# Kernel tuning notes

Hardware: AMD Instinct MI355X
Metric: run time of the kernel (lower is better)

## Reference

```python
import jax, jax.numpy as jnp
import numpy as np

B, CIN, H, W = 64, 3, 96, 96
COUT, KH, KW = 96, 5, 5
STRIDE, PAD = 2, 2
LR, K_TOP, DELTA, P_LEB = 0.02, 2, -0.4, 3.0
PREC = 1e-30


def im2col(x):
    # torch nn.Unfold ordering: channel-major (C, kh, kw) flattened -> [B, C*KH*KW, L]
    xp = jnp.pad(x, ((0, 0), (0, 0), (PAD, PAD), (PAD, PAD)))
    Hout = (H + 2 * PAD - KH) // STRIDE + 1
    Wout = (W + 2 * PAD - KW) // STRIDE + 1
    cols = []
    for i in range(KH):  # small fixed kernel loop (25 slices)
        for j in range(KW):
            cols.append(xp[:, :, i:i + STRIDE * (Hout - 1) + 1:STRIDE,
                           j:j + STRIDE * (Wout - 1) + 1:STRIDE])
    patches = jnp.stack(cols, axis=2)  # [B, C, KH*KW, Hout, Wout]
    return patches.reshape(x.shape[0], CIN * KH * KW, Hout * Wout)  # [B, K, L]


def setup_inputs() -> dict:
    key = jax.random.key(0)
    k1, k2 = jax.random.split(key)
    inp = jax.random.normal(k1, (B, CIN, H, W), dtype=jnp.float32)
    weight = jax.random.normal(k2, (COUT, CIN, KH, KW), dtype=jnp.float32)  # init.normal_
    return {"input": inp, "weight": weight}


def reference(input, weight):
    # standard conv forward (F.conv2d, no bias)
    out = jax.lax.conv_general_dilated(
        input, weight, (STRIDE, STRIDE), [(PAD, PAD), (PAD, PAD)],
        dimension_numbers=("NCHW", "OIHW", "NCHW"))

    # --- Krotov-Hopfield Hebbian update ---
    pre = im2col(input)                      # [B, K, L]
    Wm = weight.reshape(COUT, -1)            # [O, K]
    # sign(W) * |W|^(p-1) @ pre
    tot = jnp.einsum("ok,bkl->bol", jnp.sign(Wm) * jnp.abs(Wm) ** (P_LEB - 1.0), pre)  # [B,O,L]

    Bn, _, L = tot.shape
    _, idx = jax.lax.top_k(tot.transpose(0, 2, 1), K_TOP)   # [B, L, k] over output channels
    vals = jnp.concatenate([jnp.ones((1,), tot.dtype),
                            jnp.full((K_TOP - 1,), DELTA, tot.dtype)])  # top-1 -> 1.0, rest -> delta
    act = jnp.zeros((Bn, L, COUT), tot.dtype).at[
        jnp.arange(Bn)[:, None, None], jnp.arange(L)[None, :, None], idx
    ].set(jnp.broadcast_to(vals, (Bn, L, K_TOP)))
    act = act.transpose(0, 2, 1)             # [B, O, L]

    yx = jnp.einsum("bol,bkl->ok", act, pre) / L          # mean over L, sum over batch
    yy = (act * tot).sum(0).mean(1)                        # [O]
    ds = yx - yy[:, None] * Wm                             # [O, K]
    nc = jnp.maximum(jnp.max(jnp.abs(ds)), PREC)
    new_weight = weight + LR * (ds / nc).reshape(weight.shape)
    return out, new_weight
```

## Files before the change

kernel.cpp:

```cpp
#include <hip/hip_runtime.h>

#define B_     64
#define HW_    96
#define COUT_  96
#define KK_    75
#define KPAD   96
#define HOUT_  48
#define L_     2304
#define LR_    0.02f
#define DELTA_ -0.4f
#define OUT_ELEMS (B_*COUT_*L_)
#define XPITCH 100
#define XSLOTS 3368
#define C2     192
#define NPART  (B_*12)
#define ROW    (COUT_*KK_ + COUT_)
#define X2P    99
#define X2N    (33*X2P)

typedef __attribute__((ext_vector_type(8))) short short8v;
typedef __attribute__((ext_vector_type(4))) float float4v;
typedef __attribute__((ext_vector_type(4))) unsigned uint4v;

__device__ __forceinline__ unsigned short f2bf(float f) {
  unsigned u = __float_as_uint(f);
  u += 0x7fff + ((u >> 16) & 1);
  return (unsigned short)(u >> 16);
}

__device__ __forceinline__ void ins2(float v, int o, float& v1, int& o1,
                                     float& v2, int& o2) {
  bool b1 = (v > v1) || (v == v1 && o < o1);
  bool b2 = (v > v2) || (v == v2 && o < o2);
  if (b1)      { v2 = v1; o2 = o1; v1 = v; o1 = o; }
  else if (b2) { v2 = v;  o2 = o; }
}

__global__ __launch_bounds__(256) void k0_prep(const float* __restrict__ w,
                                               unsigned short* __restrict__ wbf) {
  int i = blockIdx.x * 256 + threadIdx.x;
  if (i >= 192 * KPAD) return;
  int row = i / KPAD, k = i - row * KPAD;
  float v = 0.0f;
  if (k < KK_) {
    float ww = w[(row % COUT_) * KK_ + k];
    v = (row < COUT_) ? ww : ww * fabsf(ww);
  }
  wbf[i] = f2bf(v);
}

__device__ __forceinline__ int wswz(int blk, int row) {
  return (blk < 8) ? (blk ^ (row & 7)) : (blk ^ (row & 3));
}

__global__ __launch_bounds__(256, 3) void k1_mfma(
    const float* __restrict__ x, const unsigned short* __restrict__ wbf,
    float* __restrict__ out, float4* __restrict__ top2)
{
  __shared__ __align__(16) unsigned short wlds[192 * KPAD];
  __shared__ __align__(16) float xs[XSLOTS];
  const int tid = threadIdx.x;
  const int lane = tid & 63, wq = tid >> 6;
  const int b = blockIdx.y;
  const int bx = blockIdx.x;
  const int col = lane & 15, g = lane >> 4;
  const float* xb = x + (size_t)b * (3 * HW_ * HW_);

  #pragma unroll
  for (int i = 0; i < 9; ++i) {
    int id = tid + i * 256;
    int row = id / 12, blk = id - row * 12;
    uint4v v = *(const uint4v*)(wbf + row * KPAD + blk * 8);
    *(uint4v*)((char*)wlds + row * 192 + wswz(blk, row) * 16) = v;
  }

  const int ihbase = 8 * bx - 2;
  #pragma unroll
  for (int i = 0; i < 14; ++i) {
    int idx = tid + i * 256;
    if (idx < XSLOTS) {
      int row = idx / XPITCH, iwr = idx - row * XPITCH;
      int c = row / 11, ihr = row - c * 11;
      int ih = ihbase + ihr, iw = iwr - 2;
      float v = 0.0f;
      if (c < 3 && (unsigned)ih < (unsigned)HW_ && (unsigned)iw < (unsigned)HW_)
        v = xb[(c * HW_ + ih) * HW_ + iw];
      xs[idx] = v;
    }
  }

  int offs[12][2];
  {
    const int base_fl = wq * 200 + 2 * col;
    #pragma unroll
    for (int kt = 0; kt < 3; ++kt)
      #pragma unroll
      for (int e2 = 0; e2 < 4; ++e2)
        #pragma unroll
        for (int par = 0; par < 2; ++par) {
          int k = kt * 32 + g * 8 + 2 * e2 + par;
          int c = k / 25, r = k - 25 * c, ki = r / 5, kj = r - 5 * ki;
          int fl = (k < KK_) ? base_fl + (c * 11 + ki) * XPITCH + kj
                             : 33 * XPITCH;
          offs[kt * 4 + e2][par] = fl * 4;
        }
  }

  __syncthreads();

  short8v bfr[3][3];
  #pragma unroll
  for (int nt = 0; nt < 3; ++nt)
    #pragma unroll
    for (int kt = 0; kt < 3; ++kt) {
      uint4v pk;
      #pragma unroll
      for (int e2 = 0; e2 < 4; ++e2) {
        const float* p0 = (const float*)((const char*)xs + offs[kt*4+e2][0]);
        const float* p1 = (const float*)((const char*)xs + offs[kt*4+e2][1]);
        float v0 = p0[nt * 32];
        float v1 = p1[nt * 32];
        pk[e2] = (unsigned)f2bf(v0) | ((unsigned)f2bf(v1) << 16);
      }
      bfr[nt][kt] = __builtin_bit_cast(short8v, pk);
    }

  const int lrow0 = (4 * bx + wq) * 48;
  float4v acc[3][6];

  #pragma unroll
  for (int nt = 0; nt < 3; ++nt)
    #pragma unroll
    for (int mt = 0; mt < 6; ++mt) acc[nt][mt] = (float4v)(0.0f);
  #pragma unroll
  for (int kt = 0; kt < 3; ++kt) {
    const int blk = kt * 4 + g;
    #pragma unroll
    for (int mt = 0; mt < 6; ++mt) {
      const int row = mt * 16 + col;
      short8v afr = *(const short8v*)(
          (const char*)wlds + row * 192 + wswz(blk, row) * 16);
      #pragma unroll
      for (int nt = 0; nt < 3; ++nt)
        acc[nt][mt] = __builtin_amdgcn_mfma_f32_16x16x32_bf16(
            afr, bfr[nt][kt], acc[nt][mt], 0, 0, 0);
    }
  }
  #pragma unroll
  for (int mt = 0; mt < 6; ++mt)
    #pragma unroll
    for (int r = 0; r < 4; ++r) {
      const int ch = mt * 16 + g * 4 + r;
      float* op = out + ((size_t)b * COUT_ + ch) * L_ + lrow0 + col;
      #pragma unroll
      for (int nt = 0; nt < 3; ++nt) op[nt * 16] = acc[nt][mt][r];
    }

  #pragma unroll
  for (int nt = 0; nt < 3; ++nt)
    #pragma unroll
    for (int mt = 0; mt < 6; ++mt) acc[nt][mt] = (float4v)(0.0f);
  #pragma unroll
  for (int kt = 0; kt < 3; ++kt) {
    const int blk = kt * 4 + g;
    #pragma unroll
    for (int mt = 0; mt < 6; ++mt) {
      const int row = 96 + mt * 16 + col;
      short8v afr = *(const short8v*)(
          (const char*)wlds + row * 192 + wswz(blk, row) * 16);
      #pragma unroll
      for (int nt = 0; nt < 3; ++nt)
        acc[nt][mt] = __builtin_amdgcn_mfma_f32_16x16x32_bf16(
            afr, bfr[nt][kt], acc[nt][mt], 0, 0, 0);
    }
  }
  #pragma unroll
  for (int nt = 0; nt < 3; ++nt) {
    float v1 = -3.0e38f, v2 = -3.0e38f;
    int o1 = 0x7fffffff, o2 = 0x7fffffff;
    #pragma unroll
    for (int mt = 0; mt < 6; ++mt)
      #pragma unroll
      for (int r = 0; r < 4; ++r)
        ins2(acc[nt][mt][r], mt * 16 + g * 4 + r, v1, o1, v2, o2);
    #pragma unroll
    for (int st = 0; st < 2; ++st) {
      const int d = (st == 0) ? 16 : 32;
      float bv1 = __shfl_xor(v1, d, 64);
      int   bo1 = __shfl_xor(o1, d, 64);
      float bv2 = __shfl_xor(v2, d, 64);
      int   bo2 = __shfl_xor(o2, d, 64);
      ins2(bv1, bo1, v1, o1, v2, o2);
      ins2(bv2, bo2, v1, o1, v2, o2);
    }
    if (g == 0)
      top2[(size_t)b * L_ + lrow0 + nt * 16 + col] =
          make_float4(v1, __int_as_float(o1), v2, __int_as_float(o2));
  }
}

__global__ __launch_bounds__(256, 2) void k2_gemm(
    const float* __restrict__ x, const float4* __restrict__ top2,
    float* __restrict__ part)
{
  __shared__ __align__(16) unsigned short actS[COUT_ * C2];
  __shared__ __align__(16) unsigned short preT[COUT_ * C2];
  __shared__ __align__(16) unsigned short xsb[X2N + 13];
  __shared__ float yyS[COUT_];
  const int tid = threadIdx.x;
  const int b = blockIdx.y;
  const int bx = blockIdx.x;
  const int l0 = bx * C2;
  const float* xb = x + (size_t)b * (3 * HW_ * HW_);

  {
    float4* a4 = (float4*)actS;
    #pragma unroll
    for (int i = 0; i < 9; ++i) a4[tid + i * 256] = make_float4(0, 0, 0, 0);
    float4* p4 = (float4*)((char*)preT + KK_ * (C2 * 2));
    if (tid < 252) {
      p4[2 * tid]     = make_float4(0, 0, 0, 0);
      p4[2 * tid + 1] = make_float4(0, 0, 0, 0);
    }
    if (tid < COUT_) yyS[tid] = 0.0f;
  }

  const int ihb2 = 8 * bx - 2;
  #pragma unroll
  for (int i = 0; i < 13; ++i) {
    int idx = tid + i * 256;
    if (idx < X2N) {
      int row = idx / X2P, iwr = idx - row * X2P;
      int c = row / 11, ihr = row - c * 11;
      int ih = ihb2 + ihr, iw = iwr - 2;
      float v = 0.0f;
      if (c < 3 && (unsigned)ih < (unsigned)HW_ && (unsigned)iw < (unsigned)HW_)
        v = xb[(c * HW_ + ih) * HW_ + iw];
      xsb[idx] = f2bf(v);
    }
  }
  __syncthreads();

  if (tid < C2) {
    const int pos = tid;
    const int ohr = pos / HOUT_, ow = pos - ohr * HOUT_;
    const int pblk = pos >> 3, plo = (pos & 7) << 1;
    const unsigned short* xl = xsb + (2 * ohr) * X2P + 2 * ow;
    #pragma unroll
    for (int c = 0; c < 3; ++c)
      #pragma unroll
      for (int ki = 0; ki < 5; ++ki)
        #pragma unroll
        for (int kj = 0; kj < 5; ++kj) {
          int k = c * 25 + ki * 5 + kj;
          unsigned short v = xl[(c * 11 + ki) * X2P + kj];
          *(unsigned short*)((char*)preT +
              k * (C2 * 2) + ((pblk ^ (k & 7)) << 4) + plo) = v;
        }
    float4 t2 = top2[(size_t)b * L_ + l0 + pos];
    int o1 = __float_as_int(t2.y), o2 = __float_as_int(t2.w);
    *(unsigned short*)((char*)actS +
        o1 * (C2 * 2) + ((pblk ^ (o1 & 7)) << 4) + plo) = 0x3F80;
    *(unsigned short*)((char*)actS +
        o2 * (C2 * 2) + ((pblk ^ (o2 & 7)) << 4) + plo) = f2bf(DELTA_);
    atomicAdd(&yyS[o1], t2.x);
    atomicAdd(&yyS[o2], DELTA_ * t2.z);
  }
  __syncthreads();

  const int lane = tid & 63, w = tid >> 6;
  const int col = lane & 15, g = lane >> 4;
  const int mb = (w >> 1) * 48, nb = (w & 1) * 48;

  float4v acc[3][3];
  #pragma unroll
  for (int mt = 0; mt < 3; ++mt)
    #pragma unroll
    for (int nt = 0; nt < 3; ++nt) acc[mt][nt] = (float4v)(0.0f);

  #pragma unroll
  for (int kt = 0; kt < 6; ++kt) {
    short8v a[3], bf[3];
    #pragma unroll
    for (int mt = 0; mt < 3; ++mt) {
      int row = mb + mt * 16 + col;
      a[mt] = *(const short8v*)((char*)actS + row * (C2 * 2) +
                                (((kt * 4 + g) ^ (row & 7)) << 4));
    }
    #pragma unroll
    for (int nt = 0; nt < 3; ++nt) {
      int row = nb + nt * 16 + col;
      bf[nt] = *(const short8v*)((char*)preT + row * (C2 * 2) +
                                 (((kt * 4 + g) ^ (row & 7)) << 4));
    }
    #pragma unroll
    for (int mt = 0; mt < 3; ++mt)
      #pragma unroll
      for (int nt = 0; nt < 3; ++nt)
        acc[mt][nt] = __builtin_amdgcn_mfma_f32_16x16x32_bf16(
            a[mt], bf[nt], acc[mt][nt], 0, 0, 0);
  }
  __syncthreads();

  float* prow = part + (size_t)(b * 12 + bx) * ROW;
  #pragma unroll
  for (int mt = 0; mt < 3; ++mt)
    #pragma unroll
    for (int nt = 0; nt < 3; ++nt)
      #pragma unroll
      for (int r = 0; r < 4; ++r) {
        int m = mb + mt * 16 + g * 4 + r;
        int n = nb + nt * 16 + col;
        if (n < KK_) prow[m * KK_ + n] = acc[mt][nt][r];
      }
  if (tid < COUT_) prow[COUT_ * KK_ + tid] = yyS[tid];
}

__global__ __launch_bounds__(256) void k3_reduce(
    const float* __restrict__ part, float* __restrict__ finals)
{
  __shared__ float red[4][64];
  const int e = blockIdx.x * 64 + (threadIdx.x & 63);
  const int seg = threadIdx.x >> 6;
  float s = 0.0f;
  for (int p = seg * (NPART / 4); p < (seg + 1) * (NPART / 4); ++p)
    s += part[(size_t)p * ROW + e];
  red[seg][threadIdx.x & 63] = s;
  __syncthreads();
  if (seg == 0) {
    int ll = threadIdx.x & 63;
    finals[e] = (red[0][ll] + red[1][ll]) + (red[2][ll] + red[3][ll]);
  }
}

__global__ __launch_bounds__(256) void k4_finalize(
    const float* __restrict__ w, const float* __restrict__ finals,
    float* __restrict__ outw)
{
  __shared__ float dsS[COUT_ * KK_];
  __shared__ float wmax[4];
  __shared__ float ncS;
  const int tid = threadIdx.x;
  float m = 0.0f;
  for (int i = tid; i < COUT_ * KK_; i += 256) {
    int o = i / KK_;
    float d = finals[i] - finals[COUT_ * KK_ + o] * w[i];
    dsS[i] = d;
    m = fmaxf(m, fabsf(d));
  }
  #pragma unroll
  for (int s = 32; s > 0; s >>= 1) m = fmaxf(m, __shfl_xor(m, s, 64));
  if ((tid & 63) == 0) wmax[tid >> 6] = m;
  __syncthreads();
  if (tid == 0) {
    float n = fmaxf(fmaxf(wmax[0], wmax[1]), fmaxf(wmax[2], wmax[3]));
    ncS = fmaxf(n, 1e-30f);
  }
  __syncthreads();
  const float scale = LR_ / ncS;
  for (int i = tid; i < COUT_ * KK_; i += 256) {
    outw[i] = w[i] + scale * dsS[i];
  }
}

extern "C" void kernel_launch(void* const* d_in, const int* in_sizes, int n_in,
                              void* d_out, int out_size, void* d_ws, size_t ws_size,
                              hipStream_t stream) {
  (void)in_sizes; (void)n_in; (void)out_size; (void)ws_size;
  const float* x = (const float*)d_in[0];
  const float* w = (const float*)d_in[1];
  float* out  = (float*)d_out;
  float* outw = out + OUT_ELEMS;

  unsigned short* wbf = (unsigned short*)d_ws;
  float4* top2 = (float4*)((char*)d_ws + 192 * KPAD * 2);
  float*  part = (float*)((char*)top2 + (size_t)B_ * L_ * sizeof(float4));
  float*  finals = part + (size_t)NPART * ROW;

  k0_prep   <<<dim3((192 * KPAD + 255) / 256), 256, 0, stream>>>(w, wbf);
  k1_mfma   <<<dim3(12, B_), 256, 0, stream>>>(x, wbf, out, top2);
  k2_gemm   <<<dim3(12, B_), 256, 0, stream>>>(x, top2, part);
  k3_reduce <<<dim3(ROW / 64), 256, 0, stream>>>(part, finals);
  k4_finalize<<<dim3(1), 256, 0, stream>>>(w, finals, outw);
}
```

Baseline: 115.8 us.

## Stage conv output through LDS for coalesced stores and split partial reduction

The conv output tile in k1 is now computed after the top-2 pass and transposed through shared memory (reusing the weight LDS region), so each channel row is written with contiguous float4 stores instead of scattered 4-byte stores. The partial-sum reduction is split into two kernels: a 2D grid that reduces groups of 96 partials in parallel, then a small fold kernel. This is meant to improve global write coalescing and raise parallelism in the reduction. The cost is extra barriers and LDS traffic in k1, plus one more kernel launch.

New measurement: 128.7 us. 11.1% more time.

```diff
diff --git a/kernel.cpp b/kernel.cpp
--- a/kernel.cpp
+++ b/kernel.cpp
@@ -17,6 +17,7 @@
 #define ROW    (COUT_*KK_ + COUT_)
 #define X2P    99
 #define X2N    (33*X2P)
+#define CTP    196
 
 typedef __attribute__((ext_vector_type(8))) short short8v;
 typedef __attribute__((ext_vector_type(4))) float float4v;
@@ -57,8 +58,10 @@
     const float* __restrict__ x, const unsigned short* __restrict__ wbf,
     float* __restrict__ out, float4* __restrict__ top2)
 {
-  __shared__ __align__(16) unsigned short wlds[192 * KPAD];
-  __shared__ __align__(16) float xs[XSLOTS];
+  __shared__ __align__(16) char ldsRaw[50336];
+  unsigned short* wlds = (unsigned short*)ldsRaw;
+  float* xs = (float*)(ldsRaw + 36864);
+  float* cT = (float*)ldsRaw;
   const int tid = threadIdx.x;
   const int lane = tid & 63, wq = tid >> 6;
   const int b = blockIdx.y;
@@ -137,34 +140,6 @@
     const int blk = kt * 4 + g;
     #pragma unroll
     for (int mt = 0; mt < 6; ++mt) {
-      const int row = mt * 16 + col;
-      short8v afr = *(const short8v*)(
-          (const char*)wlds + row * 192 + wswz(blk, row) * 16);
-      #pragma unroll
-      for (int nt = 0; nt < 3; ++nt)
-        acc[nt][mt] = __builtin_amdgcn_mfma_f32_16x16x32_bf16(
-            afr, bfr[nt][kt], acc[nt][mt], 0, 0, 0);
-    }
-  }
-  #pragma unroll
-  for (int mt = 0; mt < 6; ++mt)
-    #pragma unroll
-    for (int r = 0; r < 4; ++r) {
-      const int ch = mt * 16 + g * 4 + r;
-      float* op = out + ((size_t)b * COUT_ + ch) * L_ + lrow0 + col;
-      #pragma unroll
-      for (int nt = 0; nt < 3; ++nt) op[nt * 16] = acc[nt][mt][r];
-    }
-
-  #pragma unroll
-  for (int nt = 0; nt < 3; ++nt)
-    #pragma unroll
-    for (int mt = 0; mt < 6; ++mt) acc[nt][mt] = (float4v)(0.0f);
-  #pragma unroll
-  for (int kt = 0; kt < 3; ++kt) {
-    const int blk = kt * 4 + g;
-    #pragma unroll
-    for (int mt = 0; mt < 6; ++mt) {
       const int row = 96 + mt * 16 + col;
       short8v afr = *(const short8v*)(
           (const char*)wlds + row * 192 + wswz(blk, row) * 16);
@@ -196,6 +171,50 @@
     if (g == 0)
       top2[(size_t)b * L_ + lrow0 + nt * 16 + col] =
           make_float4(v1, __int_as_float(o1), v2, __int_as_float(o2));
+  }
+
+  #pragma unroll
+  for (int nt = 0; nt < 3; ++nt)
+    #pragma unroll
+    for (int mt = 0; mt < 6; ++mt) acc[nt][mt] = (float4v)(0.0f);
+  #pragma unroll
+  for (int kt = 0; kt < 3; ++kt) {
+    const int blk = kt * 4 + g;
+    #pragma unroll
+    for (int mt = 0; mt < 6; ++mt) {
+      const int row = mt * 16 + col;
+      short8v afr = *(const short8v*)(
+          (const char*)wlds + row * 192 + wswz(blk, row) * 16);
+      #pragma unroll
+      for (int nt = 0; nt < 3; ++nt)
+        acc[nt][mt] = __builtin_amdgcn_mfma_f32_16x16x32_bf16(
+            afr, bfr[nt][kt], acc[nt][mt], 0, 0, 0);
+    }
+  }
+  __syncthreads();
+
+  const int blockl = bx * 192;
+  #pragma unroll 1
+  for (int h = 0; h < 2; ++h) {
+    #pragma unroll
+    for (int mt = 0; mt < 3; ++mt)
+      #pragma unroll
+      for (int r = 0; r < 4; ++r) {
+        const int chl = mt * 16 + g * 4 + r;
+        #pragma unroll
+        for (int nt = 0; nt < 3; ++nt)
+          cT[chl * CTP + wq * 48 + nt * 16 + col] = acc[nt][h * 3 + mt][r];
+      }
+    __syncthreads();
+    const float4* cT4 = (const float4*)cT;
+    #pragma unroll
+    for (int i = 0; i < 9; ++i) {
+      int idx = tid + i * 256;
+      int ch = idx / 48, p4 = idx - ch * 48;
+      float4 v = cT4[ch * (CTP / 4) + p4];
+      *(float4*)&out[((size_t)b * COUT_ + h * 48 + ch) * L_ + blockl + 4 * p4] = v;
+    }
+    if (h == 0) __syncthreads();
   }
 }
 
@@ -316,21 +335,34 @@
   if (tid < COUT_) prow[COUT_ * KK_ + tid] = yyS[tid];
 }
 
-__global__ __launch_bounds__(256) void k3_reduce(
-    const float* __restrict__ part, float* __restrict__ finals)
+__global__ __launch_bounds__(256) void k3a_reduce(
+    const float* __restrict__ part, float* __restrict__ tmp)
 {
   __shared__ float red[4][64];
   const int e = blockIdx.x * 64 + (threadIdx.x & 63);
   const int seg = threadIdx.x >> 6;
+  const int p0 = blockIdx.y * 96 + seg * 24;
   float s = 0.0f;
-  for (int p = seg * (NPART / 4); p < (seg + 1) * (NPART / 4); ++p)
-    s += part[(size_t)p * ROW + e];
+  #pragma unroll 4
+  for (int j = 0; j < 24; ++j) s += part[(size_t)(p0 + j) * ROW + e];
   red[seg][threadIdx.x & 63] = s;
   __syncthreads();
   if (seg == 0) {
     int ll = threadIdx.x & 63;
-    finals[e] = (red[0][ll] + red[1][ll]) + (red[2][ll] + red[3][ll]);
-  }
+    tmp[(size_t)blockIdx.y * ROW + e] =
+        (red[0][ll] + red[1][ll]) + (red[2][ll] + red[3][ll]);
+  }
+}
+
+__global__ __launch_bounds__(256) void k3b_fold(
+    const float* __restrict__ tmp, float* __restrict__ finals)
+{
+  int i = blockIdx.x * 256 + threadIdx.x;
+  if (i >= ROW) return;
+  float s = 0.0f;
+  #pragma unroll
+  for (int p = 0; p < 8; ++p) s += tmp[(size_t)p * ROW + i];
+  finals[i] = s;
 }
 
 __global__ __launch_bounds__(256) void k4_finalize(
@@ -376,10 +408,12 @@
   float4* top2 = (float4*)((char*)d_ws + 192 * KPAD * 2);
   float*  part = (float*)((char*)top2 + (size_t)B_ * L_ * sizeof(float4));
   float*  finals = part + (size_t)NPART * ROW;
+  float*  tmp    = finals + ROW;
 
   k0_prep   <<<dim3((192 * KPAD + 255) / 256), 256, 0, stream>>>(w, wbf);
   k1_mfma   <<<dim3(12, B_), 256, 0, stream>>>(x, wbf, out, top2);
   k2_gemm   <<<dim3(12, B_), 256, 0, stream>>>(x, top2, part);
-  k3_reduce <<<dim3(ROW / 64), 256, 0, stream>>>(part, finals);
+  k3a_reduce<<<dim3(114, 8), 256, 0, stream>>>(part, tmp);
+  k3b_fold  <<<dim3(29), 256, 0, stream>>>(tmp, finals);
   k4_finalize<<<dim3(1), 256, 0, stream>>>(w, finals, outw);
 }
```
